# Kernel optimization log

Hardware: AMD Instinct MI355X
Metric: run time of the kernel (lower is better)

## Reference

```python
import jax, jax.numpy as jnp
import numpy as np

B, NP, NJ, ND = 16, 64, 15, 128
SIGMA = 15.0        # cfg.MULTI_PERSON.POSE_SIGMA
BIG = 1.0e5         # sentinel used to mask padded reference persons
EPS = 1e-8


def setup_inputs() -> dict:
    key = jax.random.key(0)
    k1, k2, k3, k4, k5 = jax.random.split(key, 5)
    # 3D plane-sweep hypotheses in the reference camera frame (z>0 so projection is safe)
    uv = jax.random.uniform(k1, (B, NP, NJ, ND, 2), minval=-0.5, maxval=0.5)
    z = jax.random.uniform(k2, (B, NP, NJ, ND, 1), minval=2.0, maxval=10.0)
    poses_3d = jnp.concatenate([uv * z, z], axis=-1).astype(jnp.float32)
    # detected 2D poses in the reference view, pixel coordinates
    poses_2d_ref = (jax.random.uniform(k3, (B, NP, NJ, 2)) * jnp.array([1920.0, 1080.0], jnp.float32)).astype(jnp.float32)
    vis_ref = (jax.random.uniform(k4, (B, NP, NJ)) < 0.8).astype(jnp.float32)
    num_persons_ref = jax.random.randint(k5, (B,), 1, NP + 1).astype(jnp.int32)
    R = jnp.tile(jnp.eye(3, dtype=jnp.float32), (B, 1, 1))
    T = jnp.zeros((B, 3), jnp.float32)
    f = jnp.full((B, 2), 1000.0, jnp.float32)
    c = jnp.tile(jnp.array([960.0, 540.0], jnp.float32), (B, 1))
    image_w = jnp.full((B,), 1920.0, jnp.float32)
    image_h = jnp.full((B,), 1080.0, jnp.float32)
    return dict(poses_3d=poses_3d, poses_2d_ref=poses_2d_ref, vis_ref=vis_ref,
                num_persons_ref=num_persons_ref, R=R, T=T, f=f, c=c,
                image_w=image_w, image_h=image_h)


def _project(pts, R, T, f, c):
    # pinhole projection: x_cam = R (X - T); 2d = f * xy/z + c
    xc = jnp.einsum('bij,bpkdj->bpkdi', R, pts - T[:, None, None, None, :])
    z = xc[..., 2:3]
    return f[:, None, None, None, :] * xc[..., :2] / z + c[:, None, None, None, :]


def reference(poses_3d, poses_2d_ref, vis_ref, num_persons_ref, R, T, f, c, image_w, image_h):
    # 1) project 3D hypotheses to the reference view -> [B,NP,NJ,ND,2]
    p2t = _project(poses_3d, R, T, f, c)
    # 2) visibility-weighted mean pairwise squared distance, expanded as
    #    |a|^2 + |b|^2 - 2 a.b to avoid the [B,NP,NP,NJ,ND,2] intermediate
    pt2 = jnp.sum(p2t ** 2, axis=-1)                      # [B,NP,NJ,ND]
    pr2 = jnp.sum(poses_2d_ref ** 2, axis=-1)             # [B,NQ,NJ]
    wpr = poses_2d_ref * vis_ref[..., None]               # [B,NQ,NJ,2]
    term1 = jnp.einsum('bpjd,bqj->bpqd', pt2, vis_ref)
    term2 = jnp.sum(pr2 * vis_ref, axis=-1)               # [B,NQ]
    term3 = jnp.einsum('bpjdc,bqjc->bpqd', p2t, wpr)
    vsum = jnp.sum(vis_ref, axis=-1)                      # [B,NQ]
    dist = (term1 + term2[:, None, :, None] - 2.0 * term3) / (vsum[:, None, :, None] + EPS)
    # 3) mask padded reference persons, nearest-pose matching
    valid = jnp.arange(NP)[None, :] < num_persons_ref[:, None]   # [B,NQ]
    dist = jnp.where(valid[:, None, :, None], dist, BIG)
    mm = jnp.argmin(dist, axis=2)                          # [B,NP,ND]
    # 4) gather matched 2D poses / visibilities
    b_idx = jnp.arange(B)[:, None, None]
    matched = jnp.transpose(poses_2d_ref[b_idx, mm], (0, 1, 3, 2, 4))  # [B,NP,NJ,ND,2]
    mvis = jnp.transpose(vis_ref[b_idx, mm], (0, 1, 3, 2))             # [B,NP,NJ,ND]
    # 5) exp score (non-panoptic branch) and in-image bounding
    mdist = jnp.sum((p2t - matched) ** 2, axis=-1)
    score = jnp.exp(-mdist / (SIGMA ** 2))
    iw = image_w[:, None, None, None]
    ih = image_h[:, None, None, None]
    inb = ((p2t[..., 0] >= 0) & (p2t[..., 1] >= 0) &
           (p2t[..., 0] <= iw - 1) & (p2t[..., 1] <= ih - 1)).astype(score.dtype)
    bounding = inb * mvis
    return score * bounding
```

## Files before the change

### kernel.cpp

```cpp
#include <hip/hip_runtime.h>

#define NPERS 64
#define NJOINT 15
#define NDEPTH 128
#define BIGF 100000.0f
#define EPSF 1e-8f

#define CELEM(a, j) \
    (((j) & 3) == 0 ? a[(j) >> 2].x : \
     ((j) & 3) == 1 ? a[(j) >> 2].y : \
     ((j) & 3) == 2 ? a[(j) >> 2].z : a[(j) >> 2].w)

__global__ __launch_bounds__(128, 1) void pose_match_kernel(
    const float* __restrict__ poses_3d,
    const float* __restrict__ p2d,
    const float* __restrict__ vis,
    const int*   __restrict__ nper,
    const float* __restrict__ Rm,
    const float* __restrict__ Tm,
    const float* __restrict__ fm,
    const float* __restrict__ cm,
    const float* __restrict__ iw_,
    const float* __restrict__ ih_,
    float* __restrict__ out)
{
    const int b  = blockIdx.x >> 5;
    const int pp = blockIdx.x & 31;
    const int p0 = pp * 2;
    const int d  = threadIdx.x;

    __shared__ float4 sq[NPERS][NJOINT];
    __shared__ float4 sco[NPERS][12];

    for (int i = threadIdx.x; i < NPERS * NJOINT; i += 128) {
        int q = i / NJOINT, j = i % NJOINT;
        float v  = vis[(b * NPERS + q) * NJOINT + j];
        float rx = p2d[((b * NPERS + q) * NJOINT + j) * 2 + 0];
        float ry = p2d[((b * NPERS + q) * NJOINT + j) * 2 + 1];
        sq[q][j] = make_float4(v, rx, ry, 0.0f);
    }
    __syncthreads();

    if (threadIdx.x < NPERS) {
        const int q = threadIdx.x;
        float vs = 0.0f, t2 = 0.0f;
        #pragma unroll
        for (int j = 0; j < NJOINT; ++j) {
            float4 s = sq[q][j];
            vs += s.x;
            t2 = fmaf(s.y * s.y + s.z * s.z, s.x, t2);
        }
        float inv = 1.0f / (vs + EPSF);
        float* o = (float*)&sco[q][0];
        #pragma unroll
        for (int j = 0; j < NJOINT; ++j) {
            float4 s = sq[q][j];
            o[j]      = s.x * inv;
            o[16 + j] = 2.0f * s.x * s.y * inv;
            o[32 + j] = 2.0f * s.x * s.z * inv;
        }
        o[15] = t2 * inv;
        o[31] = 0.0f;
        o[47] = 0.0f;
    }
    __syncthreads();

    const float R00 = Rm[b*9+0], R01 = Rm[b*9+1], R02 = Rm[b*9+2];
    const float R10 = Rm[b*9+3], R11 = Rm[b*9+4], R12 = Rm[b*9+5];
    const float R20 = Rm[b*9+6], R21 = Rm[b*9+7], R22 = Rm[b*9+8];
    const float T0 = Tm[b*3+0], T1 = Tm[b*3+1], T2 = Tm[b*3+2];
    const float fx = fm[b*2+0], fy = fm[b*2+1];
    const float cx = cm[b*2+0], cy = cm[b*2+1];
    const float iwm1 = iw_[b] - 1.0f;
    const float ihm1 = ih_[b] - 1.0f;
    const int   npv  = nper[b];

    float X[2][NJOINT], Y[2][NJOINT], P2[2][NJOINT];
    #pragma unroll
    for (int pi = 0; pi < 2; ++pi) {
        #pragma unroll
        for (int j = 0; j < NJOINT; ++j) {
            int base = (((b * NPERS + p0 + pi) * NJOINT + j) * NDEPTH + d) * 3;
            float a0 = poses_3d[base + 0] - T0;
            float a1 = poses_3d[base + 1] - T1;
            float a2 = poses_3d[base + 2] - T2;
            float xc0 = R00 * a0 + R01 * a1 + R02 * a2;
            float xc1 = R10 * a0 + R11 * a1 + R12 * a2;
            float xc2 = R20 * a0 + R21 * a1 + R22 * a2;
            float r   = __builtin_amdgcn_rcpf(xc2);
            float xx  = fmaf(fx * xc0, r, cx);
            float yy  = fmaf(fy * xc1, r, cy);
            X[pi][j] = xx; Y[pi][j] = yy;
            P2[pi][j] = xx * xx + yy * yy;
        }
    }

    float bestv0 = 3.0e38f, bestv1 = 3.0e38f;
    int   bestq0 = 0,       bestq1 = 0;
    #pragma unroll 2
    for (int q = 0; q < NPERS; ++q) {
        float4 cw[4], cxr[4], cyr[4];
        #pragma unroll
        for (int k = 0; k < 4; ++k) {
            cw[k]  = sco[q][k];
            cxr[k] = sco[q][4 + k];
            cyr[k] = sco[q][8 + k];
        }
        float s1a = cw[3].w, sxa = 0.0f, sya = 0.0f;
        float s1b = cw[3].w, sxb = 0.0f, syb = 0.0f;
        #pragma unroll
        for (int j = 0; j < NJOINT; ++j) {
            float w  = CELEM(cw,  j);
            float wx = CELEM(cxr, j);
            float wy = CELEM(cyr, j);
            s1a = fmaf(P2[0][j], w,  s1a);
            sxa = fmaf(X[0][j],  wx, sxa);
            sya = fmaf(Y[0][j],  wy, sya);
            s1b = fmaf(P2[1][j], w,  s1b);
            sxb = fmaf(X[1][j],  wx, sxb);
            syb = fmaf(Y[1][j],  wy, syb);
        }
        float d0 = s1a - sxa - sya;
        float d1 = s1b - sxb - syb;
        d0 = (q < npv) ? d0 : BIGF;
        d1 = (q < npv) ? d1 : BIGF;
        if (d0 < bestv0) { bestv0 = d0; bestq0 = q; }
        if (d1 < bestv1) { bestv1 = d1; bestq1 = q; }
    }

    #pragma unroll
    for (int pi = 0; pi < 2; ++pi) {
        const int bq = (pi == 0) ? bestq0 : bestq1;
        const int obase = ((b * NPERS + p0 + pi) * NJOINT) * NDEPTH + d;
        #pragma unroll
        for (int j = 0; j < NJOINT; ++j) {
            float4 v = sq[bq][j];
            float xx = X[pi][j], yy = Y[pi][j];
            float dx = xx - v.y;
            float dy = yy - v.z;
            float md = fmaf(dx, dx, dy * dy);
            float sc = __expf(-md * (1.0f / 225.0f));
            float inb = (xx >= 0.0f && yy >= 0.0f &&
                         xx <= iwm1 && yy <= ihm1) ? 1.0f : 0.0f;
            out[obase + j * NDEPTH] = sc * inb * v.x;
        }
    }
}

extern "C" void kernel_launch(void* const* d_in, const int* in_sizes, int n_in,
                              void* d_out, int out_size, void* d_ws, size_t ws_size,
                              hipStream_t stream) {
    const float* poses_3d = (const float*)d_in[0];
    const float* p2d      = (const float*)d_in[1];
    const float* vis      = (const float*)d_in[2];
    const int*   nper     = (const int*)d_in[3];
    const float* Rm       = (const float*)d_in[4];
    const float* Tm       = (const float*)d_in[5];
    const float* fm       = (const float*)d_in[6];
    const float* cm       = (const float*)d_in[7];
    const float* iw       = (const float*)d_in[8];
    const float* ih       = (const float*)d_in[9];
    float* out = (float*)d_out;

    const int B = in_sizes[3];
    dim3 grid(B * 32);
    dim3 block(128);
    pose_match_kernel<<<grid, block, 0, stream>>>(
        poses_3d, p2d, vis, nper, Rm, Tm, fm, cm, iw, ih, out);
}
```

Baseline: 32.99 us.

## Split reference-person search across four wavefronts with shared-memory argmin reduction

Blocks grow to 256 threads. Each wavefront now covers a quarter of the reference persons, and each thread handles all 4 (person, depth) combinations of its block. Partial argmins are merged through shared memory, and each wavefront then writes one (person, depth-half) slice of the output. The distance is refactored to x*(w*x - wx) form, which drops the precomputed squared-norm registers. The intent is more wavefronts per CU and less serial q-loop work per thread. The cost is redundant projection loads in every wave, higher register pressure from 60 coordinate registers, and an extra barrier.

```diff
diff --git a/kernel.cpp b/kernel.cpp
--- a/kernel.cpp
+++ b/kernel.cpp
@@ -5,13 +5,15 @@
 #define NDEPTH 128
 #define BIGF 100000.0f
 #define EPSF 1e-8f
+#define QS 4
+#define QCHUNK (NPERS / QS)
 
 #define CELEM(a, j) \
     (((j) & 3) == 0 ? a[(j) >> 2].x : \
      ((j) & 3) == 1 ? a[(j) >> 2].y : \
      ((j) & 3) == 2 ? a[(j) >> 2].z : a[(j) >> 2].w)
 
-__global__ __launch_bounds__(128, 1) void pose_match_kernel(
+__global__ __launch_bounds__(256, 2) void pose_match_kernel(
     const float* __restrict__ poses_3d,
     const float* __restrict__ p2d,
     const float* __restrict__ vis,
@@ -24,15 +26,19 @@
     const float* __restrict__ ih_,
     float* __restrict__ out)
 {
-    const int b  = blockIdx.x >> 5;
-    const int pp = blockIdx.x & 31;
-    const int p0 = pp * 2;
-    const int d  = threadIdx.x;
+    const int b    = blockIdx.x >> 5;
+    const int pp   = blockIdx.x & 31;
+    const int p0   = pp * 2;
+    const int tid  = threadIdx.x;
+    const int wv   = tid >> 6;
+    const int lane = tid & 63;
 
     __shared__ float4 sq[NPERS][NJOINT];
     __shared__ float4 sco[NPERS][12];
+    __shared__ float  bvred[QS][4][64];
+    __shared__ int    bqred[QS][4][64];
 
-    for (int i = threadIdx.x; i < NPERS * NJOINT; i += 128) {
+    for (int i = tid; i < NPERS * NJOINT; i += 256) {
         int q = i / NJOINT, j = i % NJOINT;
         float v  = vis[(b * NPERS + q) * NJOINT + j];
         float rx = p2d[((b * NPERS + q) * NJOINT + j) * 2 + 0];
@@ -41,8 +47,8 @@
     }
     __syncthreads();
 
-    if (threadIdx.x < NPERS) {
-        const int q = threadIdx.x;
+    if (tid < NPERS) {
+        const int q = tid;
         float vs = 0.0f, t2 = 0.0f;
         #pragma unroll
         for (int j = 0; j < NJOINT; ++j) {
@@ -75,30 +81,33 @@
     const float ihm1 = ih_[b] - 1.0f;
     const int   npv  = nper[b];
 
-    float X[2][NJOINT], Y[2][NJOINT], P2[2][NJOINT];
+    float X[2][2][NJOINT], Y[2][2][NJOINT];
     #pragma unroll
     for (int pi = 0; pi < 2; ++pi) {
         #pragma unroll
-        for (int j = 0; j < NJOINT; ++j) {
-            int base = (((b * NPERS + p0 + pi) * NJOINT + j) * NDEPTH + d) * 3;
-            float a0 = poses_3d[base + 0] - T0;
-            float a1 = poses_3d[base + 1] - T1;
-            float a2 = poses_3d[base + 2] - T2;
-            float xc0 = R00 * a0 + R01 * a1 + R02 * a2;
-            float xc1 = R10 * a0 + R11 * a1 + R12 * a2;
-            float xc2 = R20 * a0 + R21 * a1 + R22 * a2;
-            float r   = __builtin_amdgcn_rcpf(xc2);
-            float xx  = fmaf(fx * xc0, r, cx);
-            float yy  = fmaf(fy * xc1, r, cy);
-            X[pi][j] = xx; Y[pi][j] = yy;
-            P2[pi][j] = xx * xx + yy * yy;
+        for (int dh = 0; dh < 2; ++dh) {
+            const int d = lane + dh * 64;
+            #pragma unroll
+            for (int j = 0; j < NJOINT; ++j) {
+                int base = (((b * NPERS + p0 + pi) * NJOINT + j) * NDEPTH + d) * 3;
+                float a0 = poses_3d[base + 0] - T0;
+                float a1 = poses_3d[base + 1] - T1;
+                float a2 = poses_3d[base + 2] - T2;
+                float xc0 = R00 * a0 + R01 * a1 + R02 * a2;
+                float xc1 = R10 * a0 + R11 * a1 + R12 * a2;
+                float xc2 = R20 * a0 + R21 * a1 + R22 * a2;
+                float r   = __builtin_amdgcn_rcpf(xc2);
+                X[pi][dh][j] = fmaf(fx * xc0, r, cx);
+                Y[pi][dh][j] = fmaf(fy * xc1, r, cy);
+            }
         }
     }
 
-    float bestv0 = 3.0e38f, bestv1 = 3.0e38f;
-    int   bestq0 = 0,       bestq1 = 0;
+    float bv00 = 3.0e38f, bv01 = 3.0e38f, bv10 = 3.0e38f, bv11 = 3.0e38f;
+    int   bq00 = 0, bq01 = 0, bq10 = 0, bq11 = 0;
+    const int q0 = wv * QCHUNK;
     #pragma unroll 2
-    for (int q = 0; q < NPERS; ++q) {
+    for (int q = q0; q < q0 + QCHUNK; ++q) {
         float4 cw[4], cxr[4], cyr[4];
         #pragma unroll
         for (int k = 0; k < 4; ++k) {
@@ -106,44 +115,57 @@
             cxr[k] = sco[q][4 + k];
             cyr[k] = sco[q][8 + k];
         }
-        float s1a = cw[3].w, sxa = 0.0f, sya = 0.0f;
-        float s1b = cw[3].w, sxb = 0.0f, syb = 0.0f;
+        const float c = cw[3].w;
+        float a00 = c, a01 = c, a10 = c, a11 = c;
         #pragma unroll
         for (int j = 0; j < NJOINT; ++j) {
             float w  = CELEM(cw,  j);
             float wx = CELEM(cxr, j);
             float wy = CELEM(cyr, j);
-            s1a = fmaf(P2[0][j], w,  s1a);
-            sxa = fmaf(X[0][j],  wx, sxa);
-            sya = fmaf(Y[0][j],  wy, sya);
-            s1b = fmaf(P2[1][j], w,  s1b);
-            sxb = fmaf(X[1][j],  wx, sxb);
-            syb = fmaf(Y[1][j],  wy, syb);
+            float u;
+            u = fmaf(w, X[0][0][j], -wx); a00 = fmaf(X[0][0][j], u, a00);
+            u = fmaf(w, Y[0][0][j], -wy); a00 = fmaf(Y[0][0][j], u, a00);
+            u = fmaf(w, X[0][1][j], -wx); a01 = fmaf(X[0][1][j], u, a01);
+            u = fmaf(w, Y[0][1][j], -wy); a01 = fmaf(Y[0][1][j], u, a01);
+            u = fmaf(w, X[1][0][j], -wx); a10 = fmaf(X[1][0][j], u, a10);
+            u = fmaf(w, Y[1][0][j], -wy); a10 = fmaf(Y[1][0][j], u, a10);
+            u = fmaf(w, X[1][1][j], -wx); a11 = fmaf(X[1][1][j], u, a11);
+            u = fmaf(w, Y[1][1][j], -wy); a11 = fmaf(Y[1][1][j], u, a11);
         }
-        float d0 = s1a - sxa - sya;
-        float d1 = s1b - sxb - syb;
-        d0 = (q < npv) ? d0 : BIGF;
-        d1 = (q < npv) ? d1 : BIGF;
-        if (d0 < bestv0) { bestv0 = d0; bestq0 = q; }
-        if (d1 < bestv1) { bestv1 = d1; bestq1 = q; }
+        if (q >= npv) { a00 = BIGF; a01 = BIGF; a10 = BIGF; a11 = BIGF; }
+        if (a00 < bv00) { bv00 = a00; bq00 = q; }
+        if (a01 < bv01) { bv01 = a01; bq01 = q; }
+        if (a10 < bv10) { bv10 = a10; bq10 = q; }
+        if (a11 < bv11) { bv11 = a11; bq11 = q; }
     }
+    bvred[wv][0][lane] = bv00;  bqred[wv][0][lane] = bq00;
+    bvred[wv][1][lane] = bv01;  bqred[wv][1][lane] = bq01;
+    bvred[wv][2][lane] = bv10;  bqred[wv][2][lane] = bq10;
+    bvred[wv][3][lane] = bv11;  bqred[wv][3][lane] = bq11;
+    __syncthreads();
 
+    const int pi = wv >> 1;
+    const int dh = wv & 1;
+    float bestv = 3.0e38f;
+    int   bestq = 0;
     #pragma unroll
-    for (int pi = 0; pi < 2; ++pi) {
-        const int bq = (pi == 0) ? bestq0 : bestq1;
-        const int obase = ((b * NPERS + p0 + pi) * NJOINT) * NDEPTH + d;
-        #pragma unroll
-        for (int j = 0; j < NJOINT; ++j) {
-            float4 v = sq[bq][j];
-            float xx = X[pi][j], yy = Y[pi][j];
-            float dx = xx - v.y;
-            float dy = yy - v.z;
-            float md = fmaf(dx, dx, dy * dy);
-            float sc = __expf(-md * (1.0f / 225.0f));
-            float inb = (xx >= 0.0f && yy >= 0.0f &&
-                         xx <= iwm1 && yy <= ihm1) ? 1.0f : 0.0f;
-            out[obase + j * NDEPTH] = sc * inb * v.x;
-        }
+    for (int k = 0; k < QS; ++k) {
+        float v = bvred[k][wv][lane];
+        if (v < bestv) { bestv = v; bestq = bqred[k][wv][lane]; }
+    }
+    const int d = lane + dh * 64;
+    const int obase = ((b * NPERS + p0 + pi) * NJOINT) * NDEPTH + d;
+    #pragma unroll
+    for (int j = 0; j < NJOINT; ++j) {
+        float4 v = sq[bestq][j];
+        float xx = X[pi][dh][j], yy = Y[pi][dh][j];
+        float dx = xx - v.y;
+        float dy = yy - v.z;
+        float md = fmaf(dx, dx, dy * dy);
+        float sc = __expf(-md * (1.0f / 225.0f));
+        float inb = (xx >= 0.0f && yy >= 0.0f &&
+                     xx <= iwm1 && yy <= ihm1) ? 1.0f : 0.0f;
+        out[obase + j * NDEPTH] = sc * inb * v.x;
     }
 }
 
@@ -164,7 +186,7 @@
 
     const int B = in_sizes[3];
     dim3 grid(B * 32);
-    dim3 block(128);
+    dim3 block(256);
     pose_match_kernel<<<grid, block, 0, stream>>>(
         poses_3d, p2d, vis, nper, Rm, Tm, fm, cm, iw, ih, out);
 }
```

Result: faster. 31.23 us (-5.4%).
